# Performance work log

Hardware: AMD Instinct MI355X
Metric: run time of the kernel (lower is better)

## Reference

```python
import jax, jax.numpy as jnp
import numpy as np

B, C, D, H, W = 8, 256, 128, 64, 64


def setup_inputs() -> dict:
    key = jax.random.key(0)
    ks = jax.random.split(key, 7)
    s = 1.0 / np.sqrt(C)
    return {
        "q": jax.random.normal(ks[0], (B, C, H, W), dtype=jnp.float32),
        "k": jax.random.normal(ks[1], (B, C, H, W), dtype=jnp.float32),
        "v": jax.random.normal(ks[2], (B, C, H, W), dtype=jnp.float32),
        "W_theta": jax.random.normal(ks[3], (D, C), dtype=jnp.float32) * s,
        "W_phi": jax.random.normal(ks[4], (D, C), dtype=jnp.float32) * s,
        "W_g": jax.random.normal(ks[5], (D, C), dtype=jnp.float32) * s,
        "W_out": jax.random.normal(ks[6], (C, D), dtype=jnp.float32) * (1.0 / np.sqrt(D)),
    }


def reference(q, k, v, W_theta, W_phi, W_g, W_out):
    # 1x1 conv projections (no bias) == channel matmuls
    b, c, h, w = q.shape
    d = W_theta.shape[0]
    n = h * w
    qp = jnp.einsum('bchw,dc->bhwd', q, W_theta).reshape(b, n, d)   # [B,N,d]
    kp = jnp.einsum('bchw,dc->bhwd', k, W_phi).reshape(b, n, d)     # [B,N,d]
    vp = jnp.einsum('bchw,dc->bhwd', v, W_g).reshape(b, n, d)       # [B,N,d]
    # embedded_gaussian: scores / sqrt(d), softmax over dim=1 (query axis!)
    scores = jnp.einsum('bnd,bmd->bnm', qp, kp) / jnp.sqrt(jnp.asarray(d, qp.dtype))
    attn = jax.nn.softmax(scores, axis=1)                           # NOTE: axis=1, matches torch dim=1
    out = jnp.einsum('bnm,bmd->bnd', attn, vp).reshape(b, h, w, d)  # [B,H,W,d]
    out = jnp.einsum('bhwd,cd->bchw', out, W_out)                   # conv_out 1x1
    return v + out
```

## Files before the change

kernel.cpp:

```cpp
#include <hip/hip_runtime.h>
#include <stdint.h>

#define B_ 8
#define C_ 256
#define D_ 128
#define N_ 4096

typedef __bf16 bf16x8 __attribute__((ext_vector_type(8)));
typedef uint16_t u16x8 __attribute__((ext_vector_type(8)));
typedef uint16_t u16x4 __attribute__((ext_vector_type(4)));
typedef float f32x4 __attribute__((ext_vector_type(4)));
typedef uint32_t u32x2 __attribute__((ext_vector_type(2)));

__device__ inline uint16_t f2bf(float x) {
    union { float f; uint32_t u; } v; v.f = x;
    uint32_t u = v.u;
    return (uint16_t)((u + 0x7FFFu + ((u >> 16) & 1u)) >> 16);
}

__device__ inline float bf2f(uint16_t v) {
    union { uint32_t u; float f; } x; x.u = (uint32_t)v << 16; return x.f;
}

__device__ inline uint32_t pkbf(float lo, float hi) {
    __bf16 l = (__bf16)lo, h = (__bf16)hi;
    uint16_t lu = __builtin_bit_cast(uint16_t, l);
    uint16_t hu = __builtin_bit_cast(uint16_t, h);
    return ((uint32_t)hu << 16) | (uint32_t)lu;
}

__device__ inline float dexp2(float x) { return __builtin_amdgcn_exp2f(x); }

__global__ __launch_bounds__(256) void prep_weights(
    const float* __restrict__ wt, const float* __restrict__ wp,
    const float* __restrict__ wg, const float* __restrict__ wo,
    uint16_t* __restrict__ bwt, uint16_t* __restrict__ bwp,
    uint16_t* __restrict__ bwg, uint16_t* __restrict__ bwo)
{
    int i = blockIdx.x * 256 + threadIdx.x;
    const float scale = 0.127517431f;
    bwt[i] = f2bf(wt[i] * scale);
    bwp[i] = f2bf(wp[i]);
    bwg[i] = f2bf(wg[i]);
    bwo[i] = f2bf(wo[i]);
}

__global__ __launch_bounds__(256) void proj_kernel(
    const float* __restrict__ q, const float* __restrict__ k, const float* __restrict__ v,
    const uint16_t* __restrict__ bwt, const uint16_t* __restrict__ bwp, const uint16_t* __restrict__ bwg,
    uint16_t* __restrict__ qp, uint16_t* __restrict__ kp, uint16_t* __restrict__ vpT)
{
    const int which = blockIdx.z;
    const float* src = (which == 0) ? q : ((which == 1) ? k : v);
    const uint16_t* w = (which == 0) ? bwt : ((which == 1) ? bwp : bwg);
    const int b   = blockIdx.y;
    const int n0  = blockIdx.x * 64;
    const int wav = threadIdx.x >> 6;
    const int lane = threadIdx.x & 63;
    const int col = lane & 15;
    const int quad = lane >> 4;
    const int n = n0 + wav * 16 + col;

    const float* srcb = src + (size_t)b * C_ * N_;

    f32x4 acc[8];
#pragma unroll
    for (int mf = 0; mf < 8; ++mf) acc[mf] = (f32x4){0.f, 0.f, 0.f, 0.f};

#pragma unroll
    for (int kc = 0; kc < 8; ++kc) {
        const int cbase = kc * 32 + quad * 8;
        bf16x8 afr[8];
#pragma unroll
        for (int mf = 0; mf < 8; ++mf)
            afr[mf] = *(const bf16x8*)(w + (size_t)(mf * 16 + col) * C_ + cbase);
        float x[8];
#pragma unroll
        for (int j = 0; j < 8; ++j)
            x[j] = srcb[(size_t)(cbase + j) * N_ + n];
        u32x2 blo = (u32x2){pkbf(x[0], x[1]), pkbf(x[2], x[3])};
        u32x2 bhi = (u32x2){pkbf(x[4], x[5]), pkbf(x[6], x[7])};
        uint32_t bw[4] = {blo[0], blo[1], bhi[0], bhi[1]};
        bf16x8 bfrag = __builtin_bit_cast(bf16x8, bw);
#pragma unroll
        for (int mf = 0; mf < 8; ++mf)
            acc[mf] = __builtin_amdgcn_mfma_f32_16x16x32_bf16(afr[mf], bfrag, acc[mf], 0, 0, 0);
    }

    if (which < 2) {
        uint16_t* dst = (which == 0) ? qp : kp;
        uint16_t* base = dst + ((size_t)b * N_ + n) * D_;
#pragma unroll
        for (int mf = 0; mf < 8; ++mf) {
            u32x2 pk = (u32x2){pkbf(acc[mf][0], acc[mf][1]), pkbf(acc[mf][2], acc[mf][3])};
            *(u32x2*)(base + mf * 16 + quad * 4) = pk;
        }
    } else {
        uint16_t* base = vpT + (size_t)b * D_ * N_;
#pragma unroll
        for (int mf = 0; mf < 8; ++mf)
#pragma unroll
            for (int r = 0; r < 4; ++r) {
                int d = mf * 16 + quad * 4 + r;
                base[(size_t)d * N_ + n] = f2bf(acc[mf][r]);
            }
    }
}

__global__ __launch_bounds__(256) void pass1_denom(
    const uint16_t* __restrict__ qp, const uint16_t* __restrict__ kp,
    float* __restrict__ part)
{
    const int b  = blockIdx.x & 7;
    const int mt = (blockIdx.x >> 3) & 31;
    const int ns = blockIdx.x >> 8;
    const int m0 = mt * 128;
    const int wav = threadIdx.x >> 6;
    const int lane = threadIdx.x & 63;
    const int c = lane & 15;
    const int q = lane >> 4;

    const uint16_t* qpb = qp + (size_t)b * N_ * D_;
    const uint16_t* kpb = kp + (size_t)b * N_ * D_;

    bf16x8 bfr[8][4];
#pragma unroll
    for (int mf = 0; mf < 8; ++mf)
#pragma unroll
        for (int kc = 0; kc < 4; ++kc)
            bfr[mf][kc] = *(const bf16x8*)(kpb + (size_t)(m0 + mf * 16 + c) * D_ + kc * 32 + q * 8);

    float colsum[8];
#pragma unroll
    for (int mf = 0; mf < 8; ++mf) colsum[mf] = 0.f;

    for (int it = 0; it < 32; ++it) {
        const int nbase = ns * 2048 + it * 64 + wav * 16;
        bf16x8 afr[4];
#pragma unroll
        for (int kc = 0; kc < 4; ++kc)
            afr[kc] = *(const bf16x8*)(qpb + (size_t)(nbase + c) * D_ + kc * 32 + q * 8);
#pragma unroll
        for (int mf = 0; mf < 8; ++mf) {
            f32x4 acc = (f32x4){0.f, 0.f, 0.f, 0.f};
#pragma unroll
            for (int kc = 0; kc < 4; ++kc)
                acc = __builtin_amdgcn_mfma_f32_16x16x32_bf16(afr[kc], bfr[mf][kc], acc, 0, 0, 0);
#pragma unroll
            for (int r = 0; r < 4; ++r)
                colsum[mf] += dexp2(acc[r]);
        }
    }

    __shared__ float cs[4][128];
#pragma unroll
    for (int mf = 0; mf < 8; ++mf) {
        float s = colsum[mf];
        s += __shfl_down(s, 16, 64);
        s += __shfl_down(s, 32, 64);
        if (q == 0) cs[wav][mf * 16 + c] = s;
    }
    __syncthreads();
    if (threadIdx.x < 128) {
        float s = cs[0][threadIdx.x] + cs[1][threadIdx.x] + cs[2][threadIdx.x] + cs[3][threadIdx.x];
        part[((size_t)ns * 8 + b) * N_ + m0 + threadIdx.x] = s;
    }
}

__global__ __launch_bounds__(256) void neglog2_kernel(
    const float* __restrict__ part, float* __restrict__ l2i)
{
    int i = blockIdx.x * 256 + threadIdx.x;
    l2i[i] = -__builtin_amdgcn_logf(part[i] + part[32768 + i]);
}

__global__ __launch_bounds__(256, 2) void pass2_attn(
    const uint16_t* __restrict__ qp, const uint16_t* __restrict__ kp,
    const uint16_t* __restrict__ vpT, const float* __restrict__ l2i,
    uint16_t* __restrict__ ob0, uint16_t* __restrict__ ob1,
    uint16_t* __restrict__ ob2, uint16_t* __restrict__ ob3)
{
    const int b   = blockIdx.x & 7;
    const int qtr = (blockIdx.x >> 3) & 3;
    const int nsb = blockIdx.x >> 5;
    const int wav = threadIdx.x >> 6;
    const int lane = threadIdx.x & 63;
    const int c = lane & 15;
    const int q = lane >> 4;
    const int ntile = nsb * 256 + wav * 64;

    const uint16_t* qpb = qp + (size_t)b * N_ * D_;
    const uint16_t* kpb = kp + (size_t)b * N_ * D_;
    const uint16_t* vtb = vpT + (size_t)b * D_ * N_;
    const float* l2b = l2i + (size_t)b * N_;

    __shared__ __align__(16) uint16_t stage[2][8192];
    __shared__ __align__(16) uint16_t plds[4][4][16][72];

#define STAGE(bufidx, m0_)                                                          \
    {                                                                               \
        uint16_t* lb = &stage[bufidx][0];                                           \
        _Pragma("unroll")                                                           \
        for (int j = 0; j < 4; ++j) {                                               \
            const int fid = wav * 4 + j;                                            \
            const uint16_t* g;                                                      \
            uint16_t* ld;                                                           \
            if (fid < 8) {                                                          \
                const int P = fid * 64 + lane;                                      \
                const int mm = P >> 4, js = P & 15;                                 \
                const int jj = js ^ (mm & 7);                                       \
                g = kpb + (size_t)((m0_) + mm) * D_ + jj * 8;                       \
                ld = lb + fid * 512;                                                \
            } else {                                                                \
                const int P = (fid - 8) * 64 + lane;                                \
                const int dd = P >> 2, js = P & 3;                                  \
                const int jj = js ^ ((dd >> 1) & 3);                                \
                g = vtb + (size_t)dd * N_ + (m0_) + jj * 8;                         \
                ld = lb + 4096 + (fid - 8) * 512;                                   \
            }                                                                       \
            __builtin_amdgcn_global_load_lds(                                       \
                (const __attribute__((address_space(1))) unsigned int*)g,           \
                (__attribute__((address_space(3))) unsigned int*)ld,                \
                16, 0, 0);                                                          \
        }                                                                           \
    }

    bf16x8 qfr[4][4];
#pragma unroll
    for (int nf = 0; nf < 4; ++nf)
#pragma unroll
        for (int kc = 0; kc < 4; ++kc)
            qfr[nf][kc] = *(const bf16x8*)(qpb + (size_t)(ntile + nf * 16 + c) * D_ + kc * 32 + q * 8);

    f32x4 oacc[4][8];
#pragma unroll
    for (int nf = 0; nf < 4; ++nf)
#pragma unroll
        for (int df = 0; df < 8; ++df) oacc[nf][df] = (f32x4){0.f, 0.f, 0.f, 0.f};

    const int mstart = qtr * (N_ / 4);
    STAGE(0, mstart);
    __syncthreads();

    for (int ch = 0; ch < 32; ++ch) {
        const int m0 = mstart + ch * 32;
        const int cur = ch & 1;
        STAGE(cur ^ 1, mstart + ((ch + 1) & 31) * 32);

        const uint16_t* sb = &stage[cur][0];

        const f32x4 bias0 = *(const f32x4*)(l2b + m0 + 4 * q);
        const f32x4 bias1 = *(const f32x4*)(l2b + m0 + 16 + 4 * q);

        bf16x8 kf[2][4];
#pragma unroll
        for (int mf = 0; mf < 2; ++mf)
#pragma unroll
            for (int kc = 0; kc < 4; ++kc) {
                const int js = (kc * 4 + q) ^ (c & 7);
                kf[mf][kc] = *(const bf16x8*)(sb + (mf * 16 + c) * 128 + js * 8);
            }

        __builtin_amdgcn_s_setprio(1);
#pragma unroll
        for (int nf = 0; nf < 4; ++nf) {
            f32x4 s0 = bias0;
            f32x4 s1 = bias1;
#pragma unroll
            for (int kc = 0; kc < 4; ++kc)
                s0 = __builtin_amdgcn_mfma_f32_16x16x32_bf16(kf[0][kc], qfr[nf][kc], s0, 0, 0, 0);
#pragma unroll
            for (int kc = 0; kc < 4; ++kc)
                s1 = __builtin_amdgcn_mfma_f32_16x16x32_bf16(kf[1][kc], qfr[nf][kc], s1, 0, 0, 0);
            uint32_t p00 = pkbf(dexp2(s0[0]), dexp2(s0[1]));
            uint32_t p01 = pkbf(dexp2(s0[2]), dexp2(s0[3]));
            uint32_t p10 = pkbf(dexp2(s1[0]), dexp2(s1[1]));
            uint32_t p11 = pkbf(dexp2(s1[2]), dexp2(s1[3]));
            uint16_t* row = &plds[wav][nf][c][0];
            *(u32x2*)(row + 4 * q)      = (u32x2){p00, p01};
            *(u32x2*)(row + 16 + 4 * q) = (u32x2){p10, p11};
        }
        __builtin_amdgcn_s_setprio(0);

        const int vjs = q ^ ((c >> 1) & 3);
        bf16x8 vf[8];
#pragma unroll
        for (int df = 0; df < 8; ++df)
            vf[df] = *(const bf16x8*)(sb + 4096 + (df * 16 + c) * 32 + vjs * 8);

        bf16x8 pf[4];
#pragma unroll
        for (int nf = 0; nf < 4; ++nf)
            pf[nf] = *(const bf16x8*)(&plds[wav][nf][c][8 * q]);

        __builtin_amdgcn_s_setprio(1);
#pragma unroll
        for (int nf = 0; nf < 4; ++nf)
#pragma unroll
            for (int df = 0; df < 8; ++df)
                oacc[nf][df] = __builtin_amdgcn_mfma_f32_16x16x32_bf16(pf[nf], vf[df], oacc[nf][df], 0, 0, 0);
        __builtin_amdgcn_s_setprio(0);

        __syncthreads();
    }
#undef STAGE

    uint16_t* obq = (qtr == 0) ? ob0 : (qtr == 1) ? ob1 : (qtr == 2) ? ob2 : ob3;
#pragma unroll
    for (int nf = 0; nf < 4; ++nf) {
        uint16_t* ob = obq + ((size_t)b * N_ + ntile + nf * 16) * D_;
#pragma unroll
        for (int df = 0; df < 8; ++df)
#pragma unroll
            for (int r = 0; r < 4; ++r)
                ob[(size_t)(q * 4 + r) * D_ + df * 16 + c] = f2bf(oacc[nf][df][r]);
    }
}

__global__ __launch_bounds__(256) void pass3_out(
    const uint16_t* __restrict__ ob0, const uint16_t* __restrict__ ob1,
    const uint16_t* __restrict__ ob2, const uint16_t* __restrict__ ob3,
    const uint16_t* __restrict__ bwo,
    const float* __restrict__ v, float* __restrict__ out)
{
    const int b  = blockIdx.y;
    const int n0 = blockIdx.x * 64;
    const int wav = threadIdx.x >> 6;
    const int lane = threadIdx.x & 63;
    const int col = lane & 15;
    const int quad = lane >> 4;
    const int n = n0 + wav * 16 + col;

    const float* vb = v + (size_t)b * C_ * N_;
    float* outb = out + (size_t)b * C_ * N_;
    const size_t off = ((size_t)b * N_ + n) * D_;

    bf16x8 f0[4], f1[4], f2[4], f3[4];
#pragma unroll
    for (int kc = 0; kc < 4; ++kc) {
        f0[kc] = *(const bf16x8*)(ob0 + off + kc * 32 + quad * 8);
        f1[kc] = *(const bf16x8*)(ob1 + off + kc * 32 + quad * 8);
        f2[kc] = *(const bf16x8*)(ob2 + off + kc * 32 + quad * 8);
        f3[kc] = *(const bf16x8*)(ob3 + off + kc * 32 + quad * 8);
    }

#pragma unroll
    for (int cf = 0; cf < 16; ++cf) {
        f32x4 acc = (f32x4){0.f, 0.f, 0.f, 0.f};
#pragma unroll
        for (int kc = 0; kc < 4; ++kc) {
            bf16x8 afr = *(const bf16x8*)(bwo + (size_t)(cf * 16 + col) * D_ + kc * 32 + quad * 8);
            acc = __builtin_amdgcn_mfma_f32_16x16x32_bf16(afr, f0[kc], acc, 0, 0, 0);
            acc = __builtin_amdgcn_mfma_f32_16x16x32_bf16(afr, f1[kc], acc, 0, 0, 0);
            acc = __builtin_amdgcn_mfma_f32_16x16x32_bf16(afr, f2[kc], acc, 0, 0, 0);
            acc = __builtin_amdgcn_mfma_f32_16x16x32_bf16(afr, f3[kc], acc, 0, 0, 0);
        }
#pragma unroll
        for (int r = 0; r < 4; ++r) {
            const int cc = cf * 16 + quad * 4 + r;
            const size_t idx = (size_t)cc * N_ + n;
            outb[idx] = vb[idx] + acc[r];
        }
    }
}

extern "C" void kernel_launch(void* const* d_in, const int* in_sizes, int n_in,
                              void* d_out, int out_size, void* d_ws, size_t ws_size,
                              hipStream_t stream) {
    const float* q  = (const float*)d_in[0];
    const float* k  = (const float*)d_in[1];
    const float* v  = (const float*)d_in[2];
    const float* wt = (const float*)d_in[3];
    const float* wp = (const float*)d_in[4];
    const float* wg = (const float*)d_in[5];
    const float* wo = (const float*)d_in[6];
    float* out = (float*)d_out;

    const size_t PROJ = (size_t)B_ * N_ * D_;
    uint16_t* qp  = (uint16_t*)d_ws;
    uint16_t* kp  = qp + PROJ;
    uint16_t* vpT = kp + PROJ;
    uint16_t* ob0 = vpT + PROJ;
    uint16_t* ob1 = ob0 + PROJ;
    uint16_t* ob2 = ob1 + PROJ;
    uint16_t* ob3 = ob2 + PROJ;
    uint16_t* bwt = ob3 + PROJ;
    uint16_t* bwp = bwt + (size_t)D_ * C_;
    uint16_t* bwg = bwp + (size_t)D_ * C_;
    uint16_t* bwo = bwg + (size_t)D_ * C_;
    float* part   = (float*)(bwo + (size_t)D_ * C_);
    float* l2i    = part + (size_t)2 * 8 * N_;

    prep_weights<<<dim3(128), 256, 0, stream>>>(wt, wp, wg, wo, bwt, bwp, bwg, bwo);
    proj_kernel<<<dim3(N_ / 64, B_, 3), 256, 0, stream>>>(q, k, v, bwt, bwp, bwg, qp, kp, vpT);
    pass1_denom<<<dim3(512), 256, 0, stream>>>(qp, kp, part);
    neglog2_kernel<<<dim3(128), 256, 0, stream>>>(part, l2i);
    pass2_attn<<<dim3(512), 256, 0, stream>>>(qp, kp, vpT, l2i, ob0, ob1, ob2, ob3);
    pass3_out<<<dim3(N_ / 64, B_), 256, 0, stream>>>(ob0, ob1, ob2, ob3, bwo, v, out);
}
```

Measured before the change: 365.2 us.

## Double-buffer pass1 Q loads, remap grids by batch, skip final redundant stage

pass1_denom now software-pipelines the Q fragment loads with two register buffers so global loads overlap the MFMA/exp work. The proj, neglog2 and pass3 kernels switch to 1D grids with batch as the fastest-varying index, which changes which blocks run together and how they spread across XCDs and caches. pass2 also drops the wasted prefetch on its last chunk. Extra registers from double buffering could reduce occupancy.

```diff
diff --git a/kernel.cpp b/kernel.cpp
--- a/kernel.cpp
+++ b/kernel.cpp
@@ -50,11 +50,12 @@
     const uint16_t* __restrict__ bwt, const uint16_t* __restrict__ bwp, const uint16_t* __restrict__ bwg,
     uint16_t* __restrict__ qp, uint16_t* __restrict__ kp, uint16_t* __restrict__ vpT)
 {
-    const int which = blockIdx.z;
+    const int b = blockIdx.x & 7;
+    const int rest = blockIdx.x >> 3;
+    const int which = rest >> 6;
+    const int n0 = (rest & 63) * 64;
     const float* src = (which == 0) ? q : ((which == 1) ? k : v);
     const uint16_t* w = (which == 0) ? bwt : ((which == 1) ? bwp : bwg);
-    const int b   = blockIdx.y;
-    const int n0  = blockIdx.x * 64;
     const int wav = threadIdx.x >> 6;
     const int lane = threadIdx.x & 63;
     const int col = lane & 15;
@@ -134,23 +135,33 @@
 #pragma unroll
     for (int mf = 0; mf < 8; ++mf) colsum[mf] = 0.f;
 
-    for (int it = 0; it < 32; ++it) {
-        const int nbase = ns * 2048 + it * 64 + wav * 16;
-        bf16x8 afr[4];
-#pragma unroll
-        for (int kc = 0; kc < 4; ++kc)
-            afr[kc] = *(const bf16x8*)(qpb + (size_t)(nbase + c) * D_ + kc * 32 + q * 8);
-#pragma unroll
-        for (int mf = 0; mf < 8; ++mf) {
-            f32x4 acc = (f32x4){0.f, 0.f, 0.f, 0.f};
-#pragma unroll
-            for (int kc = 0; kc < 4; ++kc)
-                acc = __builtin_amdgcn_mfma_f32_16x16x32_bf16(afr[kc], bfr[mf][kc], acc, 0, 0, 0);
-#pragma unroll
-            for (int r = 0; r < 4; ++r)
-                colsum[mf] += dexp2(acc[r]);
-        }
-    }
+#define P1_LOAD(AFR, IT)                                                          \
+    {   const int nbase = ns * 2048 + (IT) * 64 + wav * 16;                       \
+        _Pragma("unroll")                                                         \
+        for (int kc = 0; kc < 4; ++kc)                                            \
+            AFR[kc] = *(const bf16x8*)(qpb + (size_t)(nbase + c) * D_ + kc * 32 + q * 8); }
+
+#define P1_COMPUTE(AFR)                                                           \
+    {   _Pragma("unroll")                                                         \
+        for (int mf = 0; mf < 8; ++mf) {                                          \
+            f32x4 acc = (f32x4){0.f, 0.f, 0.f, 0.f};                              \
+            _Pragma("unroll")                                                     \
+            for (int kc = 0; kc < 4; ++kc)                                        \
+                acc = __builtin_amdgcn_mfma_f32_16x16x32_bf16(AFR[kc], bfr[mf][kc], acc, 0, 0, 0); \
+            _Pragma("unroll")                                                     \
+            for (int r = 0; r < 4; ++r) colsum[mf] += dexp2(acc[r]);              \
+        } }
+
+    bf16x8 afrA[4], afrB[4];
+    P1_LOAD(afrA, 0);
+    for (int it2 = 0; it2 < 16; ++it2) {
+        P1_LOAD(afrB, 2 * it2 + 1);
+        P1_COMPUTE(afrA);
+        if (it2 < 15) P1_LOAD(afrA, 2 * it2 + 2);
+        P1_COMPUTE(afrB);
+    }
+#undef P1_LOAD
+#undef P1_COMPUTE
 
     __shared__ float cs[4][128];
 #pragma unroll
@@ -170,8 +181,10 @@
 __global__ __launch_bounds__(256) void neglog2_kernel(
     const float* __restrict__ part, float* __restrict__ l2i)
 {
-    int i = blockIdx.x * 256 + threadIdx.x;
-    l2i[i] = -__builtin_amdgcn_logf(part[i] + part[32768 + i]);
+    const int b  = blockIdx.x & 7;
+    const int m0 = (blockIdx.x >> 3) * 256;
+    const int i = b * N_ + m0 + threadIdx.x;
+    l2i[i] = -__builtin_amdgcn_logf(part[i] + part[8 * N_ + i]);
 }
 
 __global__ __launch_bounds__(256, 2) void pass2_attn(
@@ -245,7 +258,7 @@
     for (int ch = 0; ch < 32; ++ch) {
         const int m0 = mstart + ch * 32;
         const int cur = ch & 1;
-        STAGE(cur ^ 1, mstart + ((ch + 1) & 31) * 32);
+        if (ch < 31) STAGE(cur ^ 1, m0 + 32);
 
         const uint16_t* sb = &stage[cur][0];
 
@@ -323,8 +336,8 @@
     const uint16_t* __restrict__ bwo,
     const float* __restrict__ v, float* __restrict__ out)
 {
-    const int b  = blockIdx.y;
-    const int n0 = blockIdx.x * 64;
+    const int b  = blockIdx.x & 7;
+    const int n0 = (blockIdx.x >> 3) * 64;
     const int wav = threadIdx.x >> 6;
     const int lane = threadIdx.x & 63;
     const int col = lane & 15;
@@ -392,9 +405,9 @@
     float* l2i    = part + (size_t)2 * 8 * N_;
 
     prep_weights<<<dim3(128), 256, 0, stream>>>(wt, wp, wg, wo, bwt, bwp, bwg, bwo);
-    proj_kernel<<<dim3(N_ / 64, B_, 3), 256, 0, stream>>>(q, k, v, bwt, bwp, bwg, qp, kp, vpT);
+    proj_kernel<<<dim3(1536), 256, 0, stream>>>(q, k, v, bwt, bwp, bwg, qp, kp, vpT);
     pass1_denom<<<dim3(512), 256, 0, stream>>>(qp, kp, part);
     neglog2_kernel<<<dim3(128), 256, 0, stream>>>(part, l2i);
     pass2_attn<<<dim3(512), 256, 0, stream>>>(qp, kp, vpT, l2i, ob0, ob1, ob2, ob3);
-    pass3_out<<<dim3(N_ / 64, B_), 256, 0, stream>>>(ob0, ob1, ob2, ob3, bwo, v, out);
-}
+    pass3_out<<<dim3(512), 256, 0, stream>>>(ob0, ob1, ob2, ob3, bwo, v, out);
+}
```

Result: slower. 374.6 us (+2.6%).
